# Kernel tuning notes

Hardware: AMD Instinct MI355X
Metric: run time of the kernel (lower is better)

The kernel has to match this reference:

```python
import jax, jax.numpy as jnp
import numpy as np

B, L, D = 8, 2048, 1024


def setup_inputs() -> dict:
    key = jax.random.key(0)
    kq, kk, kv, km, kw1, kb1, kw2, kb2 = jax.random.split(key, 8)
    q = jax.random.normal(kq, (B, L, D), dtype=jnp.float32)
    k = jax.random.normal(kk, (B, L, D), dtype=jnp.float32)
    v = jax.random.normal(kv, (B, L, D), dtype=jnp.float32)
    attn_mask = jax.random.randint(km, (B, L, L), 0, 2).astype(bool)
    # nn.Linear(d_model, 1) params (Kaiming-uniform-ish scale)
    bound = 1.0 / np.sqrt(D)
    W1 = jax.random.uniform(kw1, (D, 1), minval=-bound, maxval=bound, dtype=jnp.float32)
    b1 = jax.random.uniform(kb1, (1,), minval=-bound, maxval=bound, dtype=jnp.float32)
    W2 = jax.random.uniform(kw2, (D, 1), minval=-bound, maxval=bound, dtype=jnp.float32)
    b2 = jax.random.uniform(kb2, (1,), minval=-bound, maxval=bound, dtype=jnp.float32)
    return {"q": q, "k": k, "v": v, "attn_mask": attn_mask,
            "W1": W1, "b1": b1, "W2": W2, "b2": b2}


def reference(q, k, v, attn_mask, W1, b1, W2, b2):
    # linear-to-scalar projections (dropout is identity in eval mode)
    q_s = (q @ W1 + b1)[..., 0]          # [B, L]
    k_s = (k @ W2 + b2)[..., 0]          # [B, L]
    # additive (concat) attention scores via broadcast add -> [B, L, L]
    attn = q_s[:, :, None] + k_s[:, None, :]
    attn = jnp.where(attn_mask, -jnp.inf, attn)
    attn = jax.nn.softmax(attn, axis=-1)
    attn = jnp.where(attn_mask, jnp.float32(0.0), attn)
    out = jnp.einsum('bls,bsd->bld', attn, v)  # bmm(attn, v)
    return out, attn
```

## Files before the change

kernel.cpp:

```cpp
#include <hip/hip_runtime.h>
#include <hip/hip_bf16.h>

#define B 8
#define L 2048
#define D 1024

typedef __bf16 bf16x8 __attribute__((ext_vector_type(8)));
typedef __bf16 bf16x4 __attribute__((ext_vector_type(4)));
typedef float f32x4 __attribute__((ext_vector_type(4)));

typedef __attribute__((address_space(3))) char lds_char;
typedef const __attribute__((address_space(1))) char glob_char;

__global__ __launch_bounds__(256) void proj_kernel(const float* __restrict__ k,
                                                   const float* __restrict__ W2,
                                                   const float* __restrict__ b2,
                                                   float* __restrict__ ks) {
    int t = threadIdx.x;
    int wave = t >> 6, lane = t & 63;
    int row = blockIdx.x * 4 + wave;
    const float4* k4 = (const float4*)(k + (size_t)row * D);
    const float4* w4 = (const float4*)W2;
    float p = 0.f;
#pragma unroll
    for (int s = 0; s < 4; s++) {
        float4 a = k4[s * 64 + lane];
        float4 w = w4[s * 64 + lane];
        p += a.x * w.x + a.y * w.y + a.z * w.z + a.w * w.w;
    }
    for (int off = 32; off > 0; off >>= 1)
        p += __shfl_down(p, off, 64);
    if (lane == 0) ks[row] = p + b2[0];
}

__global__ __launch_bounds__(256) void exp_kernel(const float* __restrict__ ks,
                                                  float* __restrict__ e) {
    int b = blockIdx.x;
    int t = threadIdx.x;
    const float* row = ks + (size_t)b * L;
    float m = -1e30f;
    for (int j = t; j < L; j += 256) m = fmaxf(m, row[j]);
    for (int off = 32; off > 0; off >>= 1)
        m = fmaxf(m, __shfl_down(m, off, 64));
    __shared__ float red[4];
    __shared__ float mb;
    int wid = t >> 6, lane = t & 63;
    if (lane == 0) red[wid] = m;
    __syncthreads();
    if (t == 0) mb = fmaxf(fmaxf(red[0], red[1]), fmaxf(red[2], red[3]));
    __syncthreads();
    float mm = mb;
    float* eo = e + (size_t)b * L;
    for (int j = t; j < L; j += 256) eo[j] = expf(row[j] - mm);
}

__global__ __launch_bounds__(256) void transpose_v(const float* __restrict__ v,
                                                   __bf16* __restrict__ vT) {
    __shared__ float tile[32][33];
    int b = blockIdx.z;
    int j0 = blockIdx.y * 32;
    int d0 = blockIdx.x * 32;
    int t = threadIdx.x;
    int jl = t >> 3;
    int dl = (t & 7) * 4;
    float4 val = *(const float4*)(v + ((size_t)b * L + j0 + jl) * D + d0 + dl);
    tile[jl][dl + 0] = val.x;
    tile[jl][dl + 1] = val.y;
    tile[jl][dl + 2] = val.z;
    tile[jl][dl + 3] = val.w;
    __syncthreads();
    int dl2 = t >> 3;
    int jl2 = (t & 7) * 4;
    bf16x4 o;
    o[0] = (__bf16)tile[jl2 + 0][dl2];
    o[1] = (__bf16)tile[jl2 + 1][dl2];
    o[2] = (__bf16)tile[jl2 + 2][dl2];
    o[3] = (__bf16)tile[jl2 + 3][dl2];
    *(bf16x4*)(vT + ((size_t)b * D + d0 + dl2) * L + j0 + jl2) = o;
}

__global__ __launch_bounds__(256) void row_kernel(const int* __restrict__ mask,
                                                  const float* __restrict__ e,
                                                  float* __restrict__ attn,
                                                  __bf16* __restrict__ P) {
    __shared__ float red[4];
    __shared__ float zsh;
    int bid = blockIdx.x;
    int b = bid >> 11;
    int t = threadIdx.x;
    const int4* m4 = (const int4*)(mask + (size_t)bid * L);
    const float4* e4 = (const float4*)(e + (size_t)b * L);
    float4 wv[2];
    float z = 0.f;
#pragma unroll
    for (int s = 0; s < 2; s++) {
        int idx = s * 256 + t;
        int4 mm = m4[idx];
        float4 ee = e4[idx];
        float4 ww;
        ww.x = mm.x ? 0.f : ee.x;
        ww.y = mm.y ? 0.f : ee.y;
        ww.z = mm.z ? 0.f : ee.z;
        ww.w = mm.w ? 0.f : ee.w;
        wv[s] = ww;
        z += ww.x + ww.y + ww.z + ww.w;
    }
    for (int off = 32; off > 0; off >>= 1)
        z += __shfl_down(z, off, 64);
    int wid = t >> 6, lane = t & 63;
    if (lane == 0) red[wid] = z;
    __syncthreads();
    if (t == 0) zsh = 1.f / (red[0] + red[1] + red[2] + red[3]);
    __syncthreads();
    float invZ = zsh;
    float4* a4 = (float4*)(attn + (size_t)bid * L);
    __bf16* prow = P + (size_t)bid * L;
#pragma unroll
    for (int s = 0; s < 2; s++) {
        int idx = s * 256 + t;
        float4 aa;
        aa.x = wv[s].x * invZ;
        aa.y = wv[s].y * invZ;
        aa.z = wv[s].z * invZ;
        aa.w = wv[s].w * invZ;
        a4[idx] = aa;
        bf16x4 pp;
        pp[0] = (__bf16)aa.x;
        pp[1] = (__bf16)aa.y;
        pp[2] = (__bf16)aa.z;
        pp[3] = (__bf16)aa.w;
        *(bf16x4*)(prow + idx * 4) = pp;
    }
}

#define BM 128
#define BN 128
#define BK 32

__global__ __launch_bounds__(256) void gemm_kernel(const __bf16* __restrict__ P,
                                                   const __bf16* __restrict__ vT,
                                                   float* __restrict__ out) {
    __shared__ __bf16 As[BM][BK];
    __shared__ __bf16 Bs[BN][BK];
    int b = blockIdx.z;
    int i0 = blockIdx.x * BM;
    int d0 = blockIdx.y * BN;
    int t = threadIdx.x;
    int wave = t >> 6, lane = t & 63;
    int wr = wave >> 1, wc = wave & 1;
    const __bf16* Ab = P + ((size_t)b * L + i0) * L;
    const __bf16* Bb = vT + ((size_t)b * D + d0) * L;

    f32x4 acc[4][4];
#pragma unroll
    for (int ti = 0; ti < 4; ti++)
#pragma unroll
        for (int tj = 0; tj < 4; tj++)
            acc[ti][tj] = (f32x4){0.f, 0.f, 0.f, 0.f};

    int lrow = lane & 15;
    int koff = (lane >> 4) * 8;

    for (int k0 = 0; k0 < L; k0 += BK) {
        __syncthreads();
#pragma unroll
        for (int s = 0; s < 2; s++) {
            int cbase = s * 256 + wave * 64;
            int c = cbase + lane;
            int r = c >> 2;
            int off = (c & 3) * 8;
            const __bf16* ga = Ab + (size_t)r * L + k0 + off;
            __builtin_amdgcn_global_load_lds((glob_char*)ga,
                                             (lds_char*)((char*)As + cbase * 16),
                                             16, 0, 0);
            const __bf16* gb = Bb + (size_t)r * L + k0 + off;
            __builtin_amdgcn_global_load_lds((glob_char*)gb,
                                             (lds_char*)((char*)Bs + cbase * 16),
                                             16, 0, 0);
        }
        __syncthreads();

        bf16x8 af[4], bfr[4];
#pragma unroll
        for (int ti = 0; ti < 4; ti++)
            af[ti] = *(const bf16x8*)&As[wr * 64 + ti * 16 + lrow][koff];
#pragma unroll
        for (int tj = 0; tj < 4; tj++)
            bfr[tj] = *(const bf16x8*)&Bs[wc * 64 + tj * 16 + lrow][koff];
#pragma unroll
        for (int ti = 0; ti < 4; ti++)
#pragma unroll
            for (int tj = 0; tj < 4; tj++)
                acc[ti][tj] = __builtin_amdgcn_mfma_f32_16x16x32_bf16(
                    af[ti], bfr[tj], acc[ti][tj], 0, 0, 0);
    }

    int col = lane & 15;
    int rquad = (lane >> 4) * 4;
#pragma unroll
    for (int ti = 0; ti < 4; ti++) {
#pragma unroll
        for (int tj = 0; tj < 4; tj++) {
#pragma unroll
            for (int r = 0; r < 4; r++) {
                int row = i0 + wr * 64 + ti * 16 + rquad + r;
                int c2 = d0 + wc * 64 + tj * 16 + col;
                out[((size_t)b * L + row) * D + c2] = acc[ti][tj][r];
            }
        }
    }
}

extern "C" void kernel_launch(void* const* d_in, const int* in_sizes, int n_in,
                              void* d_out, int out_size, void* d_ws, size_t ws_size,
                              hipStream_t stream) {
    const float* k = (const float*)d_in[1];
    const float* v = (const float*)d_in[2];
    const int* mask = (const int*)d_in[3];
    const float* W2 = (const float*)d_in[6];
    const float* b2 = (const float*)d_in[7];

    float* out = (float*)d_out;
    float* attn = out + (size_t)B * L * D;

    char* wp = (char*)d_ws;
    float* ks = (float*)wp;            wp += (size_t)B * L * 4;
    float* e = (float*)wp;             wp += (size_t)B * L * 4;
    __bf16* vT = (__bf16*)wp;          wp += (size_t)B * D * L * 2;
    __bf16* P = (__bf16*)wp;           wp += (size_t)B * L * L * 2;

    proj_kernel<<<B * L / 4, 256, 0, stream>>>(k, W2, b2, ks);
    exp_kernel<<<B, 256, 0, stream>>>(ks, e);
    transpose_v<<<dim3(D / 32, L / 32, B), 256, 0, stream>>>(v, vT);
    row_kernel<<<B * L, 256, 0, stream>>>(mask, e, attn, P);
    gemm_kernel<<<dim3(L / BM, D / BN, B), 256, 0, stream>>>(P, vT, out);
}
```

Measured before the change: 541.2 us.

## Enlarge GEMM tile to 256x128x64 and fold exp into projection kernel

The P·V GEMM block tile grows from 128x128 with BK 32 to 256x128 with BK 64. Each wave now owns a 64x128 output slab and walks two k-substeps per LDS stage, which gives more reuse per global load and fewer barriers per FLOP. The separate exp_kernel is removed: the projection now writes exp(k_s) directly without subtracting the row max, saving one launch and one pass. The price is higher register pressure and half as many GEMM blocks, plus a possible overflow if the projected scores were large.

After: 495.1 us. 8.5% less time.

```diff
diff --git a/kernel.cpp b/kernel.cpp
--- a/kernel.cpp
+++ b/kernel.cpp
@@ -15,7 +15,7 @@
 __global__ __launch_bounds__(256) void proj_kernel(const float* __restrict__ k,
                                                    const float* __restrict__ W2,
                                                    const float* __restrict__ b2,
-                                                   float* __restrict__ ks) {
+                                                   float* __restrict__ e) {
     int t = threadIdx.x;
     int wave = t >> 6, lane = t & 63;
     int row = blockIdx.x * 4 + wave;
@@ -30,28 +30,7 @@
     }
     for (int off = 32; off > 0; off >>= 1)
         p += __shfl_down(p, off, 64);
-    if (lane == 0) ks[row] = p + b2[0];
-}
-
-__global__ __launch_bounds__(256) void exp_kernel(const float* __restrict__ ks,
-                                                  float* __restrict__ e) {
-    int b = blockIdx.x;
-    int t = threadIdx.x;
-    const float* row = ks + (size_t)b * L;
-    float m = -1e30f;
-    for (int j = t; j < L; j += 256) m = fmaxf(m, row[j]);
-    for (int off = 32; off > 0; off >>= 1)
-        m = fmaxf(m, __shfl_down(m, off, 64));
-    __shared__ float red[4];
-    __shared__ float mb;
-    int wid = t >> 6, lane = t & 63;
-    if (lane == 0) red[wid] = m;
-    __syncthreads();
-    if (t == 0) mb = fmaxf(fmaxf(red[0], red[1]), fmaxf(red[2], red[3]));
-    __syncthreads();
-    float mm = mb;
-    float* eo = e + (size_t)b * L;
-    for (int j = t; j < L; j += 256) eo[j] = expf(row[j] - mm);
+    if (lane == 0) e[row] = __expf(p + b2[0]);
 }
 
 __global__ __launch_bounds__(256) void transpose_v(const float* __restrict__ v,
@@ -133,13 +112,13 @@
     }
 }
 
-#define BM 128
+#define BM 256
 #define BN 128
-#define BK 32
-
-__global__ __launch_bounds__(256) void gemm_kernel(const __bf16* __restrict__ P,
-                                                   const __bf16* __restrict__ vT,
-                                                   float* __restrict__ out) {
+#define BK 64
+
+__global__ __launch_bounds__(256, 2) void gemm_kernel(const __bf16* __restrict__ P,
+                                                      const __bf16* __restrict__ vT,
+                                                      float* __restrict__ out) {
     __shared__ __bf16 As[BM][BK];
     __shared__ __bf16 Bs[BN][BK];
     int b = blockIdx.z;
@@ -147,15 +126,14 @@
     int d0 = blockIdx.y * BN;
     int t = threadIdx.x;
     int wave = t >> 6, lane = t & 63;
-    int wr = wave >> 1, wc = wave & 1;
     const __bf16* Ab = P + ((size_t)b * L + i0) * L;
     const __bf16* Bb = vT + ((size_t)b * D + d0) * L;
 
-    f32x4 acc[4][4];
+    f32x4 acc[4][8];
 #pragma unroll
     for (int ti = 0; ti < 4; ti++)
 #pragma unroll
-        for (int tj = 0; tj < 4; tj++)
+        for (int tj = 0; tj < 8; tj++)
             acc[ti][tj] = (f32x4){0.f, 0.f, 0.f, 0.f};
 
     int lrow = lane & 15;
@@ -164,15 +142,22 @@
     for (int k0 = 0; k0 < L; k0 += BK) {
         __syncthreads();
 #pragma unroll
-        for (int s = 0; s < 2; s++) {
+        for (int s = 0; s < 8; s++) {
             int cbase = s * 256 + wave * 64;
             int c = cbase + lane;
-            int r = c >> 2;
-            int off = (c & 3) * 8;
+            int r = c >> 3;
+            int off = (c & 7) * 8;
             const __bf16* ga = Ab + (size_t)r * L + k0 + off;
             __builtin_amdgcn_global_load_lds((glob_char*)ga,
                                              (lds_char*)((char*)As + cbase * 16),
                                              16, 0, 0);
+        }
+#pragma unroll
+        for (int s = 0; s < 4; s++) {
+            int cbase = s * 256 + wave * 64;
+            int c = cbase + lane;
+            int r = c >> 3;
+            int off = (c & 7) * 8;
             const __bf16* gb = Bb + (size_t)r * L + k0 + off;
             __builtin_amdgcn_global_load_lds((glob_char*)gb,
                                              (lds_char*)((char*)Bs + cbase * 16),
@@ -180,19 +165,21 @@
         }
         __syncthreads();
 
-        bf16x8 af[4], bfr[4];
-#pragma unroll
-        for (int ti = 0; ti < 4; ti++)
-            af[ti] = *(const bf16x8*)&As[wr * 64 + ti * 16 + lrow][koff];
-#pragma unroll
-        for (int tj = 0; tj < 4; tj++)
-            bfr[tj] = *(const bf16x8*)&Bs[wc * 64 + tj * 16 + lrow][koff];
-#pragma unroll
-        for (int ti = 0; ti < 4; ti++)
-#pragma unroll
-            for (int tj = 0; tj < 4; tj++)
-                acc[ti][tj] = __builtin_amdgcn_mfma_f32_16x16x32_bf16(
-                    af[ti], bfr[tj], acc[ti][tj], 0, 0, 0);
+#pragma unroll
+        for (int kk = 0; kk < 2; kk++) {
+            bf16x8 af[4];
+#pragma unroll
+            for (int ti = 0; ti < 4; ti++)
+                af[ti] = *(const bf16x8*)&As[wave * 64 + ti * 16 + lrow][kk * 32 + koff];
+#pragma unroll
+            for (int tj = 0; tj < 8; tj++) {
+                bf16x8 bfr = *(const bf16x8*)&Bs[tj * 16 + lrow][kk * 32 + koff];
+#pragma unroll
+                for (int ti = 0; ti < 4; ti++)
+                    acc[ti][tj] = __builtin_amdgcn_mfma_f32_16x16x32_bf16(
+                        af[ti], bfr, acc[ti][tj], 0, 0, 0);
+            }
+        }
     }
 
     int col = lane & 15;
@@ -200,11 +187,11 @@
 #pragma unroll
     for (int ti = 0; ti < 4; ti++) {
 #pragma unroll
-        for (int tj = 0; tj < 4; tj++) {
+        for (int tj = 0; tj < 8; tj++) {
 #pragma unroll
             for (int r = 0; r < 4; r++) {
-                int row = i0 + wr * 64 + ti * 16 + rquad + r;
-                int c2 = d0 + wc * 64 + tj * 16 + col;
+                int row = i0 + wave * 64 + ti * 16 + rquad + r;
+                int c2 = d0 + tj * 16 + col;
                 out[((size_t)b * L + row) * D + c2] = acc[ti][tj][r];
             }
         }
@@ -224,13 +211,11 @@
     float* attn = out + (size_t)B * L * D;
 
     char* wp = (char*)d_ws;
-    float* ks = (float*)wp;            wp += (size_t)B * L * 4;
     float* e = (float*)wp;             wp += (size_t)B * L * 4;
     __bf16* vT = (__bf16*)wp;          wp += (size_t)B * D * L * 2;
     __bf16* P = (__bf16*)wp;           wp += (size_t)B * L * L * 2;
 
-    proj_kernel<<<B * L / 4, 256, 0, stream>>>(k, W2, b2, ks);
-    exp_kernel<<<B, 256, 0, stream>>>(ks, e);
+    proj_kernel<<<B * L / 4, 256, 0, stream>>>(k, W2, b2, e);
     transpose_v<<<dim3(D / 32, L / 32, B), 256, 0, stream>>>(v, vT);
     row_kernel<<<B * L, 256, 0, stream>>>(mask, e, attn, P);
     gemm_kernel<<<dim3(L / BM, D / BN, B), 256, 0, stream>>>(P, vT, out);
```
